# Optimization experiments

Hardware: AMD Instinct MI355X
Metric: run time of the kernel (lower is better)

The kernel has to match this reference:

```python
import jax, jax.numpy as jnp
import numpy as np

N, E = 50000, 800000
D_IN, D_HID, D_OUT = 256, 64, 32
LEAKY_SLOPE = 0.2  # PyG GATConv default negative_slope


def _gat(x, src, dst, W, a_src, a_dst, b, n):
    """Single-head PyG-style GATConv: gather -> edge softmax(dst) -> scatter."""
    h = x @ W                                            # [N, C]
    e = jax.nn.leaky_relu((h * a_src).sum(-1)[src] + (h * a_dst).sum(-1)[dst], LEAKY_SLOPE)  # [E]
    m = jax.ops.segment_max(e, dst, num_segments=n)      # per-dst max for stable softmax
    m = jnp.where(jnp.isfinite(m), m, 0.0)               # empty segments -> 0
    p = jnp.exp(e - m[dst])
    s = jax.ops.segment_sum(p, dst, num_segments=n)
    alpha = p / (s[dst] + 1e-16)                         # PyG softmax eps
    out = jax.ops.segment_sum(alpha[:, None] * h[src], dst, num_segments=n) + b
    return out, alpha


def setup_inputs() -> dict:
    key = jax.random.key(0)
    ks = jax.random.split(key, 16)
    g = lambda k, shape, sc: jax.random.normal(k, shape, jnp.float32) * sc
    glorot = lambda fi, fo: (2.0 / (fi + fo)) ** 0.5
    return {
        "x": g(ks[0], (N, D_IN), 1.0),
        "edge_index": jax.random.randint(ks[1], (2, E), 0, N),
        "W1": g(ks[2], (D_IN, D_HID), glorot(D_IN, D_HID)),
        "a1_src": g(ks[3], (D_HID,), 0.1),
        "a1_dst": g(ks[4], (D_HID,), 0.1),
        "b1": jnp.zeros((D_HID,), jnp.float32),
        "W2": g(ks[5], (D_HID, D_OUT), glorot(D_HID, D_OUT)),
        "a2_src": g(ks[6], (D_OUT,), 0.1),
        "a2_dst": g(ks[7], (D_OUT,), 0.1),
        "b2": jnp.zeros((D_OUT,), jnp.float32),
        "W3": g(ks[8], (D_HID, D_OUT), glorot(D_HID, D_OUT)),
        "a3_src": g(ks[9], (D_OUT,), 0.1),
        "a3_dst": g(ks[10], (D_OUT,), 0.1),
        "b3": jnp.zeros((D_OUT,), jnp.float32),
        "Wl": g(ks[11], (D_OUT, D_OUT), glorot(D_OUT, D_OUT)),
        "bl": jnp.zeros((D_OUT,), jnp.float32),
    }


def reference(x, edge_index, W1, a1_src, a1_dst, b1, W2, a2_src, a2_dst, b2,
              W3, a3_src, a3_dst, b3, Wl, bl):
    n = x.shape[0]
    src, dst = edge_index[0], edge_index[1]
    # eval mode: dropout(p=0.6) is identity
    h1, _ = _gat(x, src, dst, W1, a1_src, a1_dst, b1, n)
    h1 = jax.nn.elu(h1)
    mean, alpha = _gat(h1, src, dst, W2, a2_src, a2_dst, b2, n)
    mean = jax.nn.relu(mean)
    # conv_var uses PyG default add_self_loops=True
    loop = jnp.arange(n)
    src3 = jnp.concatenate([src, loop])
    dst3 = jnp.concatenate([dst, loop])
    var, _ = _gat(h1, src3, dst3, W3, a3_src, a3_dst, b3, n)
    mean = mean @ Wl + bl
    return mean, var, alpha
```

## Files before the change

kernel.cpp:

```cpp
#include <hip/hip_runtime.h>
#include <hip/hip_fp16.h>
#include <math.h>

#define N_NODES 50000
#define N_EDGES 800000
#define D_INF   256
#define D_HID   64
#define D_OUTF  32
#define LEAKY   0.2f

#define MT 64
#define KB 16

__device__ __forceinline__ float leaky_relu(float x){ return x >= 0.f ? x : LEAKY * x; }

union H4 { __half2 h[2]; float2 f; };
union H8 { __half2 h[4]; float4 f; };

__device__ __forceinline__ float ldg_f(const float* base, unsigned byteoff){
  return *(const float*)((const char*)base + byteoff);
}

__global__ void k_deg(const int* __restrict__ dst, int* __restrict__ deg,
                      int* __restrict__ rank){
  int i = blockIdx.x * blockDim.x + threadIdx.x;
  if (i < N_EDGES) rank[i] = atomicAdd(&deg[dst[i]], 1);
}

__global__ __launch_bounds__(256) void k_scan_a(const int* __restrict__ deg, int* __restrict__ bsum){
  __shared__ int ws[4];
  int b = blockIdx.x, t = threadIdx.x, i = b * 256 + t;
  int x = (i < N_NODES) ? deg[i] : 0;
  #pragma unroll
  for (int off = 32; off; off >>= 1) x += __shfl_down(x, off, 64);
  if ((t & 63) == 0) ws[t >> 6] = x;
  __syncthreads();
  if (t == 0) bsum[b] = ws[0] + ws[1] + ws[2] + ws[3];
}

__global__ __launch_bounds__(256) void k_scan_b(int* __restrict__ bsum, int nb,
      const float* __restrict__ W2, const float* __restrict__ W3,
      const float* __restrict__ a2s, const float* __restrict__ a2d,
      const float* __restrict__ a3s, const float* __restrict__ a3d,
      float* __restrict__ prew){
  __shared__ int ws[4];
  int t = threadIdx.x, lane = t & 63, wv = t >> 6;
  int x = (t < nb) ? bsum[t] : 0;
  #pragma unroll
  for (int off = 1; off < 64; off <<= 1){
    int y = __shfl_up(x, off, 64);
    if (lane >= off) x += y;
  }
  if (lane == 63) ws[wv] = x;
  __syncthreads();
  int add = 0;
  for (int w = 0; w < wv; ++w) add += ws[w];
  x += add;
  if (t < nb) bsum[t] = x;

  int vec = t >> 6, k = t & 63;
  const float* W = (vec < 2) ? W2 : W3;
  const float* a = (vec == 0) ? a2s : (vec == 1) ? a2d : (vec == 2) ? a3s : a3d;
  float s = 0.f;
  #pragma unroll 8
  for (int c = 0; c < D_OUTF; ++c) s = fmaf(W[k * D_OUTF + c], a[c], s);
  prew[t] = s;
}

__global__ __launch_bounds__(256) void k_scan_c(const int* __restrict__ deg,
        const int* __restrict__ bsum, int* __restrict__ rowptr){
  __shared__ int ws[4];
  int b = blockIdx.x, t = threadIdx.x, i = b * 256 + t;
  int lane = t & 63, wv = t >> 6;
  int x = (i < N_NODES) ? deg[i] : 0;
  #pragma unroll
  for (int off = 1; off < 64; off <<= 1){
    int y = __shfl_up(x, off, 64);
    if (lane >= off) x += y;
  }
  if (lane == 63) ws[wv] = x;
  __syncthreads();
  int add = (b > 0) ? bsum[b - 1] : 0;
  for (int w = 0; w < wv; ++w) add += ws[w];
  x += add;
  if (i < N_NODES) rowptr[i + 1] = x;
  if (b == 0 && t == 0) rowptr[0] = 0;
}

__global__ void k_fill(const int* __restrict__ src, const int* __restrict__ dst,
                       const int* __restrict__ rowptr, const int* __restrict__ rank,
                       int* __restrict__ srcs){
  int i = blockIdx.x * blockDim.x + threadIdx.x;
  if (i < N_EDGES){
    srcs[rowptr[dst[i]] + rank[i]] = src[i];
  }
}

__global__ __launch_bounds__(256) void k_gemm1(const float* __restrict__ x,
        const float* __restrict__ W1,
        const float* __restrict__ a_src, const float* __restrict__ a_dst,
        __half* __restrict__ h1h, float* __restrict__ es, float* __restrict__ ed){
  __shared__ float xs[2][MT][KB + 4];
  __shared__ float ws[2][KB][D_HID];
  const int tid = threadIdx.x;
  const int tc  = tid & 15;
  const int tr  = tid >> 4;
  const int row0 = blockIdx.x * MT;

  const int lxr = tid >> 2;
  const int lxp = (tid & 3) << 2;
  const int gxrow = row0 + lxr;
  const bool xok = gxrow < N_NODES;
  const float* xbase = x + (size_t)gxrow * D_INF + lxp;
  const int lwr = tid >> 4;
  const int lwp = (tid & 15) << 2;
  const float* wbase = W1 + lwr * D_HID + lwp;

  float4 xv = xok ? *(const float4*)xbase : make_float4(0.f,0.f,0.f,0.f);
  float4 wv = *(const float4*)wbase;
  *(float4*)&xs[0][lxr][lxp] = xv;
  *(float4*)&ws[0][lwr][lwp] = wv;
  __syncthreads();

  float acc[4][4] = {};
  int b = 0;
  #pragma unroll 1
  for (int ks = 0; ks < D_INF / KB; ++ks){
    if (ks < D_INF / KB - 1){
      xv = xok ? *(const float4*)(xbase + (ks + 1) * KB) : make_float4(0.f,0.f,0.f,0.f);
      wv = *(const float4*)(wbase + (size_t)(ks + 1) * KB * D_HID);
    }
    #pragma unroll
    for (int k4 = 0; k4 < KB / 4; ++k4){
      float4 xr4[4];
      #pragma unroll
      for (int r = 0; r < 4; ++r)
        xr4[r] = *(float4*)&xs[b][(tr << 2) + r][k4 << 2];
      #pragma unroll
      for (int j = 0; j < 4; ++j){
        float4 w4 = *(float4*)&ws[b][(k4 << 2) + j][tc << 2];
        #pragma unroll
        for (int r = 0; r < 4; ++r){
          float xk = (j == 0) ? xr4[r].x : (j == 1) ? xr4[r].y : (j == 2) ? xr4[r].z : xr4[r].w;
          acc[r][0] = fmaf(xk, w4.x, acc[r][0]);
          acc[r][1] = fmaf(xk, w4.y, acc[r][1]);
          acc[r][2] = fmaf(xk, w4.z, acc[r][2]);
          acc[r][3] = fmaf(xk, w4.w, acc[r][3]);
        }
      }
    }
    if (ks < D_INF / KB - 1){
      *(float4*)&xs[b ^ 1][lxr][lxp] = xv;
      *(float4*)&ws[b ^ 1][lwr][lwp] = wv;
    }
    __syncthreads();
    b ^= 1;
  }

  float as0 = a_src[tc << 2], as1 = a_src[(tc << 2) + 1],
        as2 = a_src[(tc << 2) + 2], as3 = a_src[(tc << 2) + 3];
  float ad0 = a_dst[tc << 2], ad1 = a_dst[(tc << 2) + 1],
        ad2 = a_dst[(tc << 2) + 2], ad3 = a_dst[(tc << 2) + 3];
  #pragma unroll
  for (int r = 0; r < 4; ++r){
    int row = row0 + (tr << 2) + r;
    float ps = acc[r][0]*as0 + acc[r][1]*as1 + acc[r][2]*as2 + acc[r][3]*as3;
    float pd = acc[r][0]*ad0 + acc[r][1]*ad1 + acc[r][2]*ad2 + acc[r][3]*ad3;
    #pragma unroll
    for (int off = 1; off < 16; off <<= 1){
      ps += __shfl_xor(ps, off, 64);
      pd += __shfl_xor(pd, off, 64);
    }
    if (row < N_NODES){
      H4 u;
      u.h[0] = __floats2half2_rn(acc[r][0], acc[r][1]);
      u.h[1] = __floats2half2_rn(acc[r][2], acc[r][3]);
      *(float2*)&h1h[(size_t)row * D_HID + (tc << 2)] = u.f;
      if (tc == 0){ es[row] = ps; ed[row] = pd; }
    }
  }
}

__global__ __launch_bounds__(256) void k_agg1(const int* __restrict__ rowptr,
      const int* __restrict__ srcs, const __half* __restrict__ h1,
      const float* __restrict__ es, const float* __restrict__ ed,
      const float* __restrict__ b1, __half* __restrict__ h1act){
  int t = threadIdx.x, lane = t & 63, wv = t >> 6;
  int slot = lane >> 3, cg = lane & 7;
  unsigned coff = cg << 4;

  int node = blockIdx.x * 4 + wv;
  int beg = rowptr[node], end = rowptr[node + 1];
  float edv = ed[node];
  float4 aL = {0,0,0,0}, aH = {0,0,0,0};
  float ss = 0.f;
  for (int i = beg; i < end; i += 32){
    int sA[4]; float4 vr[4]; float p[4];
    #pragma unroll
    for (int u = 0; u < 4; ++u){
      int idx = i + (u << 3) + slot;
      sA[u] = srcs[idx < end ? idx : end - 1];
    }
    #pragma unroll
    for (int u = 0; u < 4; ++u)
      vr[u] = *(const float4*)((const char*)h1 + ((unsigned)sA[u] << 7) + coff);
    #pragma unroll
    for (int u = 0; u < 4; ++u){
      float e = __expf(leaky_relu(ldg_f(es, (unsigned)sA[u] << 2) + edv));
      p[u] = ((i + (u << 3) + slot) < end) ? e : 0.f;
    }
    #pragma unroll
    for (int u = 0; u < 4; ++u){
      ss += p[u];
      H8 hh; hh.f = vr[u];
      float2 c0 = __half22float2(hh.h[0]);
      float2 c1 = __half22float2(hh.h[1]);
      float2 c2 = __half22float2(hh.h[2]);
      float2 c3 = __half22float2(hh.h[3]);
      aL.x = fmaf(p[u], c0.x, aL.x); aL.y = fmaf(p[u], c0.y, aL.y);
      aL.z = fmaf(p[u], c1.x, aL.z); aL.w = fmaf(p[u], c1.y, aL.w);
      aH.x = fmaf(p[u], c2.x, aH.x); aH.y = fmaf(p[u], c2.y, aH.y);
      aH.z = fmaf(p[u], c3.x, aH.z); aH.w = fmaf(p[u], c3.y, aH.w);
    }
  }
  #pragma unroll
  for (int off = 8; off <= 32; off <<= 1){
    aL.x += __shfl_xor(aL.x, off, 64); aL.y += __shfl_xor(aL.y, off, 64);
    aL.z += __shfl_xor(aL.z, off, 64); aL.w += __shfl_xor(aL.w, off, 64);
    aH.x += __shfl_xor(aH.x, off, 64); aH.y += __shfl_xor(aH.y, off, 64);
    aH.z += __shfl_xor(aH.z, off, 64); aH.w += __shfl_xor(aH.w, off, 64);
    ss   += __shfl_xor(ss,   off, 64);
  }
  if (slot == 0){
    float inv = 1.f / (ss + 1e-16f);
    int ch0 = cg << 3;
    float4 bA = *(const float4*)&b1[ch0];
    float4 bB = *(const float4*)&b1[ch0 + 4];
    float v0 = aL.x * inv + bA.x; v0 = v0 > 0.f ? v0 : expm1f(v0);
    float v1 = aL.y * inv + bA.y; v1 = v1 > 0.f ? v1 : expm1f(v1);
    float v2 = aL.z * inv + bA.z; v2 = v2 > 0.f ? v2 : expm1f(v2);
    float v3 = aL.w * inv + bA.w; v3 = v3 > 0.f ? v3 : expm1f(v3);
    float v4 = aH.x * inv + bB.x; v4 = v4 > 0.f ? v4 : expm1f(v4);
    float v5 = aH.y * inv + bB.y; v5 = v5 > 0.f ? v5 : expm1f(v5);
    float v6 = aH.z * inv + bB.z; v6 = v6 > 0.f ? v6 : expm1f(v6);
    float v7 = aH.w * inv + bB.w; v7 = v7 > 0.f ? v7 : expm1f(v7);
    H8 o;
    o.h[0] = __floats2half2_rn(v0, v1);
    o.h[1] = __floats2half2_rn(v2, v3);
    o.h[2] = __floats2half2_rn(v4, v5);
    o.h[3] = __floats2half2_rn(v6, v7);
    *(float4*)&h1act[(size_t)node * D_HID + ch0] = o.f;
  }
}

__global__ __launch_bounds__(256) void k_gemm23(const __half* __restrict__ h1acth,
        const float* __restrict__ W2, const float* __restrict__ W3,
        const float* __restrict__ prew,
        __half* __restrict__ h23h, float2* __restrict__ es23,
        float2* __restrict__ edinv2, float* __restrict__ ed3){
  __shared__ float hs[64][68];
  __shared__ float wsd[64][64];
  __shared__ float sprew[256];
  const int tid = threadIdx.x;
  const int row0 = blockIdx.x * 64;

  {
    int r = tid >> 2, cg = tid & 3;
    int grow = row0 + r;
    bool ok = grow < N_NODES;
    const float4* hrow = (const float4*)(h1acth + (size_t)grow * D_HID + cg * 16);
    H8 q0, q1;
    q0.f = ok ? hrow[0] : make_float4(0,0,0,0);
    q1.f = ok ? hrow[1] : make_float4(0,0,0,0);
    float* dsth = &hs[r][cg * 16];
    #pragma unroll
    for (int j = 0; j < 4; ++j){
      float2 f = __half22float2(q0.h[j]);
      dsth[j * 2] = f.x; dsth[j * 2 + 1] = f.y;
    }
    #pragma unroll
    for (int j = 0; j < 4; ++j){
      float2 f = __half22float2(q1.h[j]);
      dsth[8 + j * 2] = f.x; dsth[8 + j * 2 + 1] = f.y;
    }
    int k = tid >> 2;
    const float* Wsrc = (cg < 2) ? W2 : W3;
    int cbase = (cg & 1) * 16;
    float4* dstw = (float4*)&wsd[k][cg * 16];
    const float4* srcw = (const float4*)&Wsrc[k * D_OUTF + cbase];
    #pragma unroll
    for (int j = 0; j < 4; ++j) dstw[j] = srcw[j];
    sprew[tid] = prew[tid];
  }
  __syncthreads();

  {
    int r = tid >> 2, q = tid & 3, row = row0 + r;
    float d0 = 0.f, d1 = 0.f, d2 = 0.f, d3 = 0.f;
    #pragma unroll
    for (int k = 0; k < 16; ++k){
      float hval = hs[r][(q << 4) + k];
      d0 = fmaf(hval, sprew[(q << 4) + k], d0);
      d1 = fmaf(hval, sprew[64 + (q << 4) + k], d1);
      d2 = fmaf(hval, sprew[128 + (q << 4) + k], d2);
      d3 = fmaf(hval, sprew[192 + (q << 4) + k], d3);
    }
    #pragma unroll
    for (int off = 1; off < 4; off <<= 1){
      d0 += __shfl_xor(d0, off, 64);
      d1 += __shfl_xor(d1, off, 64);
      d2 += __shfl_xor(d2, off, 64);
      d3 += __shfl_xor(d3, off, 64);
    }
    if (q == 0 && row < N_NODES){
      es23[row] = make_float2(d0, d2);
      edinv2[row].x = d1;
      ed3[row] = d3;
    }
  }

  const int tc = tid & 15, tr = tid >> 4;
  float acc[4][4] = {};
  #pragma unroll
  for (int k4 = 0; k4 < 16; ++k4){
    float4 xr4[4];
    #pragma unroll
    for (int r = 0; r < 4; ++r)
      xr4[r] = *(float4*)&hs[(tr << 2) + r][k4 << 2];
    #pragma unroll
    for (int j = 0; j < 4; ++j){
      float4 w4 = *(float4*)&wsd[(k4 << 2) + j][tc << 2];
      #pragma unroll
      for (int r = 0; r < 4; ++r){
        float xk = (j == 0) ? xr4[r].x : (j == 1) ? xr4[r].y : (j == 2) ? xr4[r].z : xr4[r].w;
        acc[r][0] = fmaf(xk, w4.x, acc[r][0]);
        acc[r][1] = fmaf(xk, w4.y, acc[r][1]);
        acc[r][2] = fmaf(xk, w4.z, acc[r][2]);
        acc[r][3] = fmaf(xk, w4.w, acc[r][3]);
      }
    }
  }
  #pragma unroll
  for (int r = 0; r < 4; ++r){
    int row = row0 + (tr << 2) + r;
    if (row < N_NODES){
      H4 u;
      u.h[0] = __floats2half2_rn(acc[r][0], acc[r][1]);
      u.h[1] = __floats2half2_rn(acc[r][2], acc[r][3]);
      *(float2*)&h23h[(size_t)row * 64 + (tc << 2)] = u.f;
    }
  }
}

__global__ __launch_bounds__(256) void k_agg23(const int* __restrict__ rowptr,
   const int* __restrict__ srcs, const __half* __restrict__ h23,
   const float2* __restrict__ es23, float2* __restrict__ edinv2,
   const float* __restrict__ ed3,
   const float* __restrict__ b2, const float* __restrict__ b3,
   const float* __restrict__ Wlin, const float* __restrict__ blin,
   float* __restrict__ mean_out, float* __restrict__ var_out){
  __shared__ float sWl[D_OUTF * D_OUTF];
  int t = threadIdx.x, lane = t & 63, wv = t >> 6;
  int slot = lane >> 3, cg = lane & 7;
  int layer = cg >> 2;
  unsigned coff = cg << 4;
  for (int idx = t; idx < D_OUTF * D_OUTF; idx += 256) sWl[idx] = Wlin[idx];
  __syncthreads();

  int node = blockIdx.x * 4 + wv;
  int beg = rowptr[node], end = rowptr[node + 1];
  float edv = layer ? ed3[node] : edinv2[node].x;
  float4 aL = {0,0,0,0}, aH = {0,0,0,0};
  float ss = 0.f;
  for (int i = beg; i < end; i += 32){
    int sA[4]; float4 vr[4]; float p[4];
    #pragma unroll
    for (int u = 0; u < 4; ++u){
      int idx = i + (u << 3) + slot;
      sA[u] = srcs[idx < end ? idx : end - 1];
    }
    #pragma unroll
    for (int u = 0; u < 4; ++u)
      vr[u] = *(const float4*)((const char*)h23 + ((unsigned)sA[u] << 7) + coff);
    #pragma unroll
    for (int u = 0; u < 4; ++u){
      float2 e2 = *(const float2*)((const char*)es23 + ((unsigned)sA[u] << 3));
      float esv = layer ? e2.y : e2.x;
      float e = __expf(leaky_relu(esv + edv));
      p[u] = ((i + (u << 3) + slot) < end) ? e : 0.f;
    }
    #pragma unroll
    for (int u = 0; u < 4; ++u){
      ss += p[u];
      H8 hh; hh.f = vr[u];
      float2 c0 = __half22float2(hh.h[0]);
      float2 c1 = __half22float2(hh.h[1]);
      float2 c2 = __half22float2(hh.h[2]);
      float2 c3 = __half22float2(hh.h[3]);
      aL.x = fmaf(p[u], c0.x, aL.x); aL.y = fmaf(p[u], c0.y, aL.y);
      aL.z = fmaf(p[u], c1.x, aL.z); aL.w = fmaf(p[u], c1.y, aL.w);
      aH.x = fmaf(p[u], c2.x, aH.x); aH.y = fmaf(p[u], c2.y, aH.y);
      aH.z = fmaf(p[u], c3.x, aH.z); aH.w = fmaf(p[u], c3.y, aH.w);
    }
  }
  #pragma unroll
  for (int off = 8; off <= 32; off <<= 1){
    aL.x += __shfl_xor(aL.x, off, 64); aL.y += __shfl_xor(aL.y, off, 64);
    aL.z += __shfl_xor(aL.z, off, 64); aL.w += __shfl_xor(aL.w, off, 64);
    aH.x += __shfl_xor(aH.x, off, 64); aH.y += __shfl_xor(aH.y, off, 64);
    aH.z += __shfl_xor(aH.z, off, 64); aH.w += __shfl_xor(aH.w, off, 64);
    ss   += __shfl_xor(ss,   off, 64);
  }

  {
    float psr = __expf(leaky_relu(es23[node].y + ed3[node]));
    float psg = layer ? psr : 0.f;
    H8 hh; hh.f = *(const float4*)((const char*)h23 + ((unsigned)node << 7) + coff);
    float2 c0 = __half22float2(hh.h[0]);
    float2 c1 = __half22float2(hh.h[1]);
    float2 c2 = __half22float2(hh.h[2]);
    float2 c3 = __half22float2(hh.h[3]);
    aL.x = fmaf(psg, c0.x, aL.x); aL.y = fmaf(psg, c0.y, aL.y);
    aL.z = fmaf(psg, c1.x, aL.z); aL.w = fmaf(psg, c1.y, aL.w);
    aH.x = fmaf(psg, c2.x, aH.x); aH.y = fmaf(psg, c2.y, aH.y);
    aH.z = fmaf(psg, c3.x, aH.z); aH.w = fmaf(psg, c3.y, aH.w);
    ss += psg;
  }
  float inv = 1.f / (ss + 1e-16f);

  float m0=0,m1=0,m2=0,m3=0,m4=0,m5=0,m6=0,m7=0;
  if (!layer){
    int ch0 = cg << 3;
    float4 bA = *(const float4*)&b2[ch0];
    float4 bB = *(const float4*)&b2[ch0 + 4];
    m0 = aL.x * inv + bA.x; m0 = m0 > 0.f ? m0 : 0.f;
    m1 = aL.y * inv + bA.y; m1 = m1 > 0.f ? m1 : 0.f;
    m2 = aL.z * inv + bA.z; m2 = m2 > 0.f ? m2 : 0.f;
    m3 = aL.w * inv + bA.w; m3 = m3 > 0.f ? m3 : 0.f;
    m4 = aH.x * inv + bB.x; m4 = m4 > 0.f ? m4 : 0.f;
    m5 = aH.y * inv + bB.y; m5 = m5 > 0.f ? m5 : 0.f;
    m6 = aH.z * inv + bB.z; m6 = m6 > 0.f ? m6 : 0.f;
    m7 = aH.w * inv + bB.w; m7 = m7 > 0.f ? m7 : 0.f;
  } else if (slot == 0){
    int ch0 = (cg & 3) << 3;
    float4 bA = *(const float4*)&b3[ch0];
    float4 bB = *(const float4*)&b3[ch0 + 4];
    float4 oA = { aL.x * inv + bA.x, aL.y * inv + bA.y, aL.z * inv + bA.z, aL.w * inv + bA.w };
    float4 oB = { aH.x * inv + bB.x, aH.y * inv + bB.y, aH.z * inv + bB.z, aH.w * inv + bB.w };
    *(float4*)&var_out[(size_t)node * D_OUTF + ch0]     = oA;
    *(float4*)&var_out[(size_t)node * D_OUTF + ch0 + 4] = oB;
  }

  {
    int c = lane & 31;
    float o = blin[c];
    #pragma unroll
    for (int cgs = 0; cgs < 4; ++cgs){
      float q0 = __shfl(m0, cgs, 64), q1 = __shfl(m1, cgs, 64);
      float q2 = __shfl(m2, cgs, 64), q3 = __shfl(m3, cgs, 64);
      float q4 = __shfl(m4, cgs, 64), q5 = __shfl(m5, cgs, 64);
      float q6 = __shfl(m6, cgs, 64), q7 = __shfl(m7, cgs, 64);
      int j0 = cgs << 3;
      o = fmaf(q0, sWl[(j0+0) * D_OUTF + c], o);
      o = fmaf(q1, sWl[(j0+1) * D_OUTF + c], o);
      o = fmaf(q2, sWl[(j0+2) * D_OUTF + c], o);
      o = fmaf(q3, sWl[(j0+3) * D_OUTF + c], o);
      o = fmaf(q4, sWl[(j0+4) * D_OUTF + c], o);
      o = fmaf(q5, sWl[(j0+5) * D_OUTF + c], o);
      o = fmaf(q6, sWl[(j0+6) * D_OUTF + c], o);
      o = fmaf(q7, sWl[(j0+7) * D_OUTF + c], o);
    }
    if (lane < 32) mean_out[(size_t)node * D_OUTF + c] = o;
  }
  if (lane == 0) edinv2[node].y = inv;
}

__global__ __launch_bounds__(256) void k_alpha(const int* __restrict__ src,
    const int* __restrict__ dst,
    const float2* __restrict__ es23, const float2* __restrict__ edinv2,
    float* __restrict__ alpha_out){
  int e = blockIdx.x * blockDim.x + threadIdx.x;
  if (e < N_EDGES){
    int s = src[e], d = dst[e];
    float2 ei = *(const float2*)((const char*)edinv2 + ((unsigned)d << 3));
    float esv = ((const float2*)((const char*)es23 + ((unsigned)s << 3)))->x;
    alpha_out[e] = __expf(leaky_relu(esv + ei.x)) * ei.y;
  }
}

extern "C" void kernel_launch(void* const* d_in, const int* in_sizes, int n_in,
                              void* d_out, int out_size, void* d_ws, size_t ws_size,
                              hipStream_t stream) {
  const float* x   = (const float*)d_in[0];
  const int*   ei  = (const int*)d_in[1];
  const int*   src = ei;
  const int*   dst = ei + N_EDGES;
  const float* W1  = (const float*)d_in[2];
  const float* a1s = (const float*)d_in[3];
  const float* a1d = (const float*)d_in[4];
  const float* b1  = (const float*)d_in[5];
  const float* W2  = (const float*)d_in[6];
  const float* a2s = (const float*)d_in[7];
  const float* a2d = (const float*)d_in[8];
  const float* b2  = (const float*)d_in[9];
  const float* W3  = (const float*)d_in[10];
  const float* a3s = (const float*)d_in[11];
  const float* a3d = (const float*)d_in[12];
  const float* b3  = (const float*)d_in[13];
  const float* Wl  = (const float*)d_in[14];
  const float* bl  = (const float*)d_in[15];

  float* out       = (float*)d_out;
  float* mean_out  = out;
  float* var_out   = out + (size_t)N_NODES * D_OUTF;
  float* alpha_out = out + 2 * (size_t)N_NODES * D_OUTF;

  const int NSCAN = (N_NODES + 255) / 256;

  int* deg      = (int*)d_ws;
  int* rowptr   = deg + N_NODES;
  int* bsum     = rowptr + (N_NODES + 1);
  int* rank     = bsum + NSCAN;
  int* srcs     = rank + N_EDGES;
  size_t ioff   = (size_t)((srcs + N_EDGES) - (int*)d_ws);
  ioff = (ioff + 3) & ~(size_t)3;
  __half* h1    = (__half*)((int*)d_ws + ioff);
  __half* h1act = h1 + (size_t)N_NODES * 64;
  __half* h23   = h1act + (size_t)N_NODES * 64;
  float* es1    = (float*)(h23 + (size_t)N_NODES * 64);
  float* ed1    = es1 + N_NODES;
  float* ed3    = ed1 + N_NODES;
  float* prew   = ed3 + N_NODES;
  float2* es23  = (float2*)(prew + 256);
  float2* edinv2= es23 + N_NODES;

  hipMemsetAsync(deg, 0, (size_t)N_NODES * sizeof(int), stream);

  k_deg   <<<(N_EDGES + 255) / 256, 256, 0, stream>>>(dst, deg, rank);
  k_scan_a<<<NSCAN, 256, 0, stream>>>(deg, bsum);
  k_scan_b<<<1, 256, 0, stream>>>(bsum, NSCAN, W2, W3, a2s, a2d, a3s, a3d, prew);
  k_scan_c<<<NSCAN, 256, 0, stream>>>(deg, bsum, rowptr);
  k_fill  <<<(N_EDGES + 255) / 256, 256, 0, stream>>>(src, dst, rowptr, rank, srcs);

  k_gemm1<<<(N_NODES + MT - 1) / MT, 256, 0, stream>>>(x, W1, a1s, a1d, h1, es1, ed1);
  k_agg1 <<<N_NODES / 4, 256, 0, stream>>>(rowptr, srcs, h1, es1, ed1, b1, h1act);
  k_gemm23<<<(N_NODES + 63) / 64, 256, 0, stream>>>(h1act, W2, W3, prew,
                                                    h23, es23, edinv2, ed3);
  k_agg23<<<N_NODES / 4, 256, 0, stream>>>(rowptr, srcs, h23, es23, edinv2, ed3,
                                           b2, b3, Wl, bl, mean_out, var_out);
  k_alpha<<<(N_EDGES + 255) / 256, 256, 0, stream>>>(src, dst, es23, edinv2, alpha_out);
}
```

Baseline: 212.5 us.

## Process two destination nodes per wavefront in aggregation kernels

Each 64-lane wavefront in the two edge-aggregation kernels now splits into two 32-lane halves, each handling its own destination node with 4 edge slots per iteration instead of 8. With an average degree of 16, the old layout left many lanes masked on the 32-edge stride; the new one sizes the stride to about one node's edges and halves the grid. The cost is divergence, since the loop runs to the larger degree of the two paired nodes, and the final lane shuffles and the output projection must be remapped per half.

Measured after the change: 190.4 us. 10.4% less time.

```diff
diff --git a/kernel.cpp b/kernel.cpp
--- a/kernel.cpp
+++ b/kernel.cpp
@@ -186,20 +186,25 @@
       const float* __restrict__ es, const float* __restrict__ ed,
       const float* __restrict__ b1, __half* __restrict__ h1act){
   int t = threadIdx.x, lane = t & 63, wv = t >> 6;
-  int slot = lane >> 3, cg = lane & 7;
+  int nh = lane >> 5, sub = lane & 31;
+  int slot2 = sub >> 3, cg = sub & 7;
   unsigned coff = cg << 4;
 
-  int node = blockIdx.x * 4 + wv;
+  int node = blockIdx.x * 8 + wv * 2 + nh;
   int beg = rowptr[node], end = rowptr[node + 1];
+  int len = end - beg;
+  int lenO = __shfl_xor(len, 32, 64);
+  int lenmax = len > lenO ? len : lenO;
+  int fallback = (len > 0) ? end - 1 : 0;
   float edv = ed[node];
   float4 aL = {0,0,0,0}, aH = {0,0,0,0};
   float ss = 0.f;
-  for (int i = beg; i < end; i += 32){
+  for (int off = 0; off < lenmax; off += 16){
     int sA[4]; float4 vr[4]; float p[4];
     #pragma unroll
     for (int u = 0; u < 4; ++u){
-      int idx = i + (u << 3) + slot;
-      sA[u] = srcs[idx < end ? idx : end - 1];
+      int idx = beg + off + (u << 2) + slot2;
+      sA[u] = srcs[idx < end ? idx : fallback];
     }
     #pragma unroll
     for (int u = 0; u < 4; ++u)
@@ -207,7 +212,7 @@
     #pragma unroll
     for (int u = 0; u < 4; ++u){
       float e = __expf(leaky_relu(ldg_f(es, (unsigned)sA[u] << 2) + edv));
-      p[u] = ((i + (u << 3) + slot) < end) ? e : 0.f;
+      p[u] = ((off + (u << 2) + slot2) < len) ? e : 0.f;
     }
     #pragma unroll
     for (int u = 0; u < 4; ++u){
@@ -224,14 +229,14 @@
     }
   }
   #pragma unroll
-  for (int off = 8; off <= 32; off <<= 1){
+  for (int off = 8; off <= 16; off <<= 1){
     aL.x += __shfl_xor(aL.x, off, 64); aL.y += __shfl_xor(aL.y, off, 64);
     aL.z += __shfl_xor(aL.z, off, 64); aL.w += __shfl_xor(aL.w, off, 64);
     aH.x += __shfl_xor(aH.x, off, 64); aH.y += __shfl_xor(aH.y, off, 64);
     aH.z += __shfl_xor(aH.z, off, 64); aH.w += __shfl_xor(aH.w, off, 64);
     ss   += __shfl_xor(ss,   off, 64);
   }
-  if (slot == 0){
+  if (slot2 == 0){
     float inv = 1.f / (ss + 1e-16f);
     int ch0 = cg << 3;
     float4 bA = *(const float4*)&b1[ch0];
@@ -361,23 +366,28 @@
    float* __restrict__ mean_out, float* __restrict__ var_out){
   __shared__ float sWl[D_OUTF * D_OUTF];
   int t = threadIdx.x, lane = t & 63, wv = t >> 6;
-  int slot = lane >> 3, cg = lane & 7;
+  int nh = lane >> 5, sub = lane & 31;
+  int slot2 = sub >> 3, cg = sub & 7;
   int layer = cg >> 2;
   unsigned coff = cg << 4;
   for (int idx = t; idx < D_OUTF * D_OUTF; idx += 256) sWl[idx] = Wlin[idx];
   __syncthreads();
 
-  int node = blockIdx.x * 4 + wv;
+  int node = blockIdx.x * 8 + wv * 2 + nh;
   int beg = rowptr[node], end = rowptr[node + 1];
+  int len = end - beg;
+  int lenO = __shfl_xor(len, 32, 64);
+  int lenmax = len > lenO ? len : lenO;
+  int fallback = (len > 0) ? end - 1 : 0;
   float edv = layer ? ed3[node] : edinv2[node].x;
   float4 aL = {0,0,0,0}, aH = {0,0,0,0};
   float ss = 0.f;
-  for (int i = beg; i < end; i += 32){
+  for (int off = 0; off < lenmax; off += 16){
     int sA[4]; float4 vr[4]; float p[4];
     #pragma unroll
     for (int u = 0; u < 4; ++u){
-      int idx = i + (u << 3) + slot;
-      sA[u] = srcs[idx < end ? idx : end - 1];
+      int idx = beg + off + (u << 2) + slot2;
+      sA[u] = srcs[idx < end ? idx : fallback];
     }
     #pragma unroll
     for (int u = 0; u < 4; ++u)
@@ -387,7 +397,7 @@
       float2 e2 = *(const float2*)((const char*)es23 + ((unsigned)sA[u] << 3));
       float esv = layer ? e2.y : e2.x;
       float e = __expf(leaky_relu(esv + edv));
-      p[u] = ((i + (u << 3) + slot) < end) ? e : 0.f;
+      p[u] = ((off + (u << 2) + slot2) < len) ? e : 0.f;
     }
     #pragma unroll
     for (int u = 0; u < 4; ++u){
@@ -404,7 +414,7 @@
     }
   }
   #pragma unroll
-  for (int off = 8; off <= 32; off <<= 1){
+  for (int off = 8; off <= 16; off <<= 1){
     aL.x += __shfl_xor(aL.x, off, 64); aL.y += __shfl_xor(aL.y, off, 64);
     aL.z += __shfl_xor(aL.z, off, 64); aL.w += __shfl_xor(aL.w, off, 64);
     aH.x += __shfl_xor(aH.x, off, 64); aH.y += __shfl_xor(aH.y, off, 64);
@@ -441,7 +451,7 @@
     m5 = aH.y * inv + bB.y; m5 = m5 > 0.f ? m5 : 0.f;
     m6 = aH.z * inv + bB.z; m6 = m6 > 0.f ? m6 : 0.f;
     m7 = aH.w * inv + bB.w; m7 = m7 > 0.f ? m7 : 0.f;
-  } else if (slot == 0){
+  } else if (slot2 == 0){
     int ch0 = (cg & 3) << 3;
     float4 bA = *(const float4*)&b3[ch0];
     float4 bB = *(const float4*)&b3[ch0 + 4];
@@ -452,14 +462,16 @@
   }
 
   {
-    int c = lane & 31;
+    int c = sub;
+    int lbase = lane & 32;
     float o = blin[c];
     #pragma unroll
     for (int cgs = 0; cgs < 4; ++cgs){
-      float q0 = __shfl(m0, cgs, 64), q1 = __shfl(m1, cgs, 64);
-      float q2 = __shfl(m2, cgs, 64), q3 = __shfl(m3, cgs, 64);
-      float q4 = __shfl(m4, cgs, 64), q5 = __shfl(m5, cgs, 64);
-      float q6 = __shfl(m6, cgs, 64), q7 = __shfl(m7, cgs, 64);
+      int sl = lbase | cgs;
+      float q0 = __shfl(m0, sl, 64), q1 = __shfl(m1, sl, 64);
+      float q2 = __shfl(m2, sl, 64), q3 = __shfl(m3, sl, 64);
+      float q4 = __shfl(m4, sl, 64), q5 = __shfl(m5, sl, 64);
+      float q6 = __shfl(m6, sl, 64), q7 = __shfl(m7, sl, 64);
       int j0 = cgs << 3;
       o = fmaf(q0, sWl[(j0+0) * D_OUTF + c], o);
       o = fmaf(q1, sWl[(j0+1) * D_OUTF + c], o);
@@ -470,9 +482,9 @@
       o = fmaf(q6, sWl[(j0+6) * D_OUTF + c], o);
       o = fmaf(q7, sWl[(j0+7) * D_OUTF + c], o);
     }
-    if (lane < 32) mean_out[(size_t)node * D_OUTF + c] = o;
-  }
-  if (lane == 0) edinv2[node].y = inv;
+    mean_out[(size_t)node * D_OUTF + c] = o;
+  }
+  if (sub == 0) edinv2[node].y = inv;
 }
 
 __global__ __launch_bounds__(256) void k_alpha(const int* __restrict__ src,
@@ -543,10 +555,10 @@
   k_fill  <<<(N_EDGES + 255) / 256, 256, 0, stream>>>(src, dst, rowptr, rank, srcs);
 
   k_gemm1<<<(N_NODES + MT - 1) / MT, 256, 0, stream>>>(x, W1, a1s, a1d, h1, es1, ed1);
-  k_agg1 <<<N_NODES / 4, 256, 0, stream>>>(rowptr, srcs, h1, es1, ed1, b1, h1act);
+  k_agg1 <<<N_NODES / 8, 256, 0, stream>>>(rowptr, srcs, h1, es1, ed1, b1, h1act);
   k_gemm23<<<(N_NODES + 63) / 64, 256, 0, stream>>>(h1act, W2, W3, prew,
                                                     h23, es23, edinv2, ed3);
-  k_agg23<<<N_NODES / 4, 256, 0, stream>>>(rowptr, srcs, h23, es23, edinv2, ed3,
+  k_agg23<<<N_NODES / 8, 256, 0, stream>>>(rowptr, srcs, h23, es23, edinv2, ed3,
                                            b2, b3, Wl, bl, mean_out, var_out);
   k_alpha<<<(N_EDGES + 255) / 256, 256, 0, stream>>>(src, dst, es23, edinv2, alpha_out);
 }
```
